# Kernel optimization log

Hardware: AMD Instinct MI355X
Metric: run time of the kernel (lower is better)

Reference implementation:

```python
import jax, jax.numpy as jnp
import numpy as np

N, E, D, H, C = 50000, 1600000, 256, 8, 32

def setup_inputs() -> dict:
    key = jax.random.key(0)
    ks = jax.random.split(key, 7)
    feat = jax.random.normal(ks[0], (N, D), dtype=jnp.float32)
    edge_weight = jax.random.uniform(ks[1], (E,), dtype=jnp.float32)
    W_lin = jax.random.normal(ks[2], (D, H * C), dtype=jnp.float32) * (1.0 / np.sqrt(D))
    att_l = jax.random.normal(ks[3], (1, H, C), dtype=jnp.float32) * (1.0 / np.sqrt(H))
    att_r = jax.random.normal(ks[4], (1, H, C), dtype=jnp.float32) * (1.0 / np.sqrt(H))
    W_res = jax.random.normal(ks[5], (D, H * C), dtype=jnp.float32) * (1.0 / np.sqrt(D))
    edge_index = jax.random.randint(ks[6], (2, E), 0, N, dtype=jnp.int32)
    return {"feat": feat, "edge_weight": edge_weight, "W_lin": W_lin,
            "att_l": att_l, "att_r": att_r, "W_res": W_res, "edge_index": edge_index}

def reference(feat, edge_weight, W_lin, att_l, att_r, W_res, edge_index):
    n_nodes = feat.shape[0]
    h, c = att_l.shape[1], att_l.shape[2]
    src, dst = edge_index[0], edge_index[1]
    # node projection: [N, H, C]
    x = (feat @ W_lin).reshape(n_nodes, h, c)
    alpha_l = (x * att_l).sum(-1)  # [N, H]
    alpha_r = (x * att_r).sum(-1)  # [N, H]
    # per-edge scores [E, H]
    alpha = alpha_l[src] + alpha_r[dst]
    alpha = edge_weight[:, None] * alpha
    alpha = jnp.where(alpha > 0, alpha, 0.2 * alpha)  # leaky_relu(0.2)
    # segment softmax over destination nodes
    amax = jax.lax.stop_gradient(jax.ops.segment_max(alpha, dst, num_segments=n_nodes))
    ex = jnp.exp(alpha - amax[dst])
    denom = jax.ops.segment_sum(ex, dst, num_segments=n_nodes)
    coeff = ex / (denom[dst] + 1e-16)  # [E, H]
    # weighted message aggregation
    msg = x[src] * coeff[:, :, None]  # [E, H, C]
    agg = jax.ops.segment_sum(msg, dst, num_segments=n_nodes)  # [N, H, C]
    out = jax.nn.elu(agg).reshape(n_nodes, h * c)
    out = out + feat @ W_res  # residual
    return out
```

## Files before the change

### kernel.cpp

```cpp
#include <hip/hip_runtime.h>
#include <stdint.h>

#define D_DIM 256
#define NPAD  640

typedef __bf16 bf16x8 __attribute__((ext_vector_type(8)));
typedef float  f32x4  __attribute__((ext_vector_type(4)));

__device__ __forceinline__ float bf2f(unsigned short u) {
  union { unsigned int i; float f; } cv; cv.i = ((unsigned int)u) << 16; return cv.f;
}
__device__ __forceinline__ unsigned short f2bf(float f) {
  union { float f; unsigned int i; } cv; cv.f = f;
  unsigned int i = cv.i;
  unsigned int lsb = (i >> 16) & 1u;
  i += 0x7fffu + lsb;
  return (unsigned short)(i >> 16);
}
__device__ __forceinline__ void gld16(const void* gptr, void* lptr) {
  __builtin_amdgcn_global_load_lds(
      (const __attribute__((address_space(1))) unsigned int*)gptr,
      (__attribute__((address_space(3))) unsigned int*)lptr, 16, 0, 0);
}

__global__ __launch_bounds__(256) void setup_cvt_prep(
    const float* __restrict__ feat, unsigned short* __restrict__ fb,
    const float* __restrict__ W_lin, const float* __restrict__ W_res,
    const float* __restrict__ att_l, const float* __restrict__ att_r,
    unsigned short* __restrict__ Bt, int nelem, int nb_cvt) {
  int bid = blockIdx.x, t = threadIdx.x;
  if (bid < nb_cvt) {
    int i = (bid * 256 + t) * 8;
    if (i >= nelem) return;
    float4 v0 = *(const float4*)(feat + i);
    float4 v1 = *(const float4*)(feat + i + 4);
    ushort4 a, b;
    a.x = f2bf(v0.x); a.y = f2bf(v0.y); a.z = f2bf(v0.z); a.w = f2bf(v0.w);
    b.x = f2bf(v1.x); b.y = f2bf(v1.y); b.z = f2bf(v1.z); b.w = f2bf(v1.w);
    *(ushort4*)(fb + i) = a;
    *(ushort4*)(fb + i + 4) = b;
  } else {
    int idx = (bid - nb_cvt) * 256 + t;
    int n = idx >> 8, k = idx & 255;
    float v = 0.f;
    if (n < 256) v = W_lin[k * 256 + n];
    else if (n < 512) v = W_res[k * 256 + (n - 256)];
    else if (n < 520) {
      int h = n - 512; float s = 0.f;
      #pragma unroll
      for (int c = 0; c < 32; ++c) s += W_lin[k * 256 + h * 32 + c] * att_l[h * 32 + c];
      v = s;
    } else if (n < 528) {
      int h = n - 520; float s = 0.f;
      #pragma unroll
      for (int c = 0; c < 32; ++c) s += W_lin[k * 256 + h * 32 + c] * att_r[h * 32 + c];
      v = s;
    }
    Bt[idx] = f2bf(v);
  }
}

__global__ __launch_bounds__(256) void scan_partial(const int* __restrict__ cnt,
                                                    int* __restrict__ bsum, int N) {
  __shared__ int s[256];
  int t = threadIdx.x;
  int i = blockIdx.x * 256 + t;
  s[t] = (i < N) ? cnt[i] : 0;
  __syncthreads();
  for (int off = 128; off > 0; off >>= 1) {
    if (t < off) s[t] += s[t + off];
    __syncthreads();
  }
  if (t == 0) bsum[blockIdx.x] = s[0];
}

__global__ __launch_bounds__(256) void scan_top(int* __restrict__ bsum, int nb) {
  __shared__ int s[256];
  int t = threadIdx.x;
  int v = (t < nb) ? bsum[t] : 0;
  s[t] = v;
  __syncthreads();
  for (int off = 1; off < 256; off <<= 1) {
    int u = (t >= off) ? s[t - off] : 0;
    __syncthreads();
    s[t] += u;
    __syncthreads();
  }
  if (t < nb) bsum[t] = s[t] - v;
}

__global__ __launch_bounds__(256) void scan_apply(const int* __restrict__ cnt,
                                                  const int* __restrict__ bsum,
                                                  int* __restrict__ row_ptr, int N) {
  __shared__ int s[256];
  int t = threadIdx.x;
  int i = blockIdx.x * 256 + t;
  int v = (i < N) ? cnt[i] : 0;
  s[t] = v;
  __syncthreads();
  for (int off = 1; off < 256; off <<= 1) {
    int u = (t >= off) ? s[t - off] : 0;
    __syncthreads();
    s[t] += u;
    __syncthreads();
  }
  int excl = bsum[blockIdx.x] + s[t] - v;
  if (i < N) {
    row_ptr[i] = excl;
    if (i == N - 1) row_ptr[N] = excl + v;
  }
}

__global__ __launch_bounds__(256) void gemm_hist(
    const unsigned short* __restrict__ A,
    const unsigned short* __restrict__ Bt,
    float* __restrict__ out, unsigned short* __restrict__ xbf,
    float* __restrict__ alpha_l, float* __restrict__ alpha_r, int M,
    const int* __restrict__ dst, int* __restrict__ cnt, int* __restrict__ rank,
    int E, int nb_hist, int gx) {
  __shared__ unsigned short As[128 * 64];
  __shared__ unsigned short Bs[128 * 64];

  if ((int)blockIdx.x < nb_hist) {
    int base = (int)blockIdx.x * 2048 + threadIdx.x;
    #pragma unroll
    for (int u = 0; u < 8; ++u) {
      int e = base + u * 256;
      if (e < E) rank[e] = atomicAdd(&cnt[dst[e]], 1);
    }
    return;
  }

  int tid  = threadIdx.x;
  int w    = tid >> 6, lane = tid & 63;
  int gb   = (int)blockIdx.x - nb_hist;
  int bm   = (gb % gx) * 128, bn = (gb / gx) * 128;
  int wm   = (w & 1) * 64, wn = (w >> 1) * 64;
  int l16  = lane & 15, quad = lane >> 4;

  f32x4 acc[4][4] = {};

  int sr8     = lane >> 3;
  int koff_sw = (((lane & 7) ^ sr8) * 8);

  for (int k0 = 0; k0 < 256; k0 += 64) {
    #pragma unroll
    for (int j = 0; j < 4; ++j) {
      int rbase = w * 32 + j * 8;
      int rga = bm + rbase + sr8; if (rga > M - 1) rga = M - 1;
      gld16(A  + (size_t)rga * 256 + k0 + koff_sw, &As[rbase * 64]);
      gld16(Bt + (size_t)(bn + rbase + sr8) * 256 + k0 + koff_sw, &Bs[rbase * 64]);
    }
    __syncthreads();
    #pragma unroll
    for (int kk = 0; kk < 64; kk += 32) {
      bf16x8 a[4], b[4];
      #pragma unroll
      for (int mi = 0; mi < 4; ++mi) {
        int r = wm + mi * 16 + l16;
        int col = (kk * 2 + quad * 16) ^ ((r & 7) << 4);
        a[mi] = *(const bf16x8*)((const char*)&As[r * 64] + col);
      }
      #pragma unroll
      for (int ni = 0; ni < 4; ++ni) {
        int r = wn + ni * 16 + l16;
        int col = (kk * 2 + quad * 16) ^ ((r & 7) << 4);
        b[ni] = *(const bf16x8*)((const char*)&Bs[r * 64] + col);
      }
      #pragma unroll
      for (int mi = 0; mi < 4; ++mi)
        #pragma unroll
        for (int ni = 0; ni < 4; ++ni)
          acc[mi][ni] = __builtin_amdgcn_mfma_f32_16x16x32_bf16(a[mi], b[ni], acc[mi][ni], 0, 0, 0);
    }
    __syncthreads();
  }

  #pragma unroll
  for (int mi = 0; mi < 4; ++mi) {
    #pragma unroll
    for (int r = 0; r < 4; ++r) {
      int row = bm + wm + mi * 16 + quad * 4 + r;
      if (row >= M) continue;
      #pragma unroll
      for (int ni = 0; ni < 4; ++ni) {
        int n = bn + wn + ni * 16 + l16;
        float v = acc[mi][ni][r];
        if (n < 256)      xbf[(size_t)row * 256 + n] = f2bf(v);
        else if (n < 512) out[(size_t)row * 256 + (n - 256)] = v;
        else if (n < 520) alpha_l[row * 8 + (n - 512)] = v;
        else if (n < 528) alpha_r[row * 8 + (n - 520)] = v;
      }
    }
  }
}

__global__ __launch_bounds__(256) void scatter_kernel(
    const int* __restrict__ eidx, const float* __restrict__ ew,
    const int* __restrict__ row_ptr, const int* __restrict__ rank,
    int2* __restrict__ pairs, int E) {
  int e = blockIdx.x * 256 + threadIdx.x;
  if (e < E) {
    int d = eidx[E + e];
    int pos = row_ptr[d] + rank[e];
    int2 p; p.x = eidx[e]; p.y = __float_as_int(ew[e]);
    pairs[pos] = p;
  }
}

__global__ __launch_bounds__(256) void agg_kernel(
    const int* __restrict__ row_ptr, const int2* __restrict__ pairs,
    const float* __restrict__ alpha_l, const float* __restrict__ alpha_r,
    const unsigned short* __restrict__ xbf, float* __restrict__ out, int N) {
  __shared__ float red[2][64][6];
  int nin  = threadIdx.x >> 7;
  int wv   = (threadIdx.x >> 6) & 1;
  int lane = threadIdx.x & 63;
  int node = blockIdx.x * 2 + nin;
  bool active = node < N;
  int h  = lane >> 3;
  int cb = lane << 2;

  float l = 0.f, ac0 = 0.f, ac1 = 0.f, ac2 = 0.f, ac3 = 0.f;

  if (active) {
    int beg = row_ptr[node], end = row_ptr[node + 1];
    if (beg < end) {
      float arv = alpha_r[node * 8 + h];
      int last = end - 1;
      const unsigned short* xb = xbf + cb;
      for (int jg = beg + wv * 4; jg < end; jg += 8) {
        int2 q[4];
        #pragma unroll
        for (int u = 0; u < 4; ++u) {
          int t = jg + u; t = (t < last) ? t : last;
          q[u] = pairs[t];
        }
        float al[4];
        #pragma unroll
        for (int u = 0; u < 4; ++u) al[u] = alpha_l[(size_t)q[u].x * 8 + h];
        ushort4 xv[4];
        #pragma unroll
        for (int u = 0; u < 4; ++u)
          xv[u] = *(const ushort4*)(xb + ((size_t)q[u].x << 8));
        #pragma unroll
        for (int u = 0; u < 4; ++u) {
          float a = __int_as_float(q[u].y) * (al[u] + arv);
          a = (a > 0.f) ? a : 0.2f * a;
          float p = __expf(a);
          p = (jg + u < end) ? p : 0.f;
          l += p;
          ac0 = fmaf(p, bf2f(xv[u].x), ac0);
          ac1 = fmaf(p, bf2f(xv[u].y), ac1);
          ac2 = fmaf(p, bf2f(xv[u].z), ac2);
          ac3 = fmaf(p, bf2f(xv[u].w), ac3);
        }
      }
    }
  }

  if (wv == 1) {
    red[nin][lane][0] = l;
    red[nin][lane][1] = ac0; red[nin][lane][2] = ac1;
    red[nin][lane][3] = ac2; red[nin][lane][4] = ac3;
  }
  __syncthreads();
  if (active && wv == 0) {
    l   += red[nin][lane][0];
    ac0 += red[nin][lane][1]; ac1 += red[nin][lane][2];
    ac2 += red[nin][lane][3]; ac3 += red[nin][lane][4];
    float r = 1.0f / (l + 1e-16f);
    float o0 = ac0 * r, o1 = ac1 * r, o2 = ac2 * r, o3 = ac3 * r;
    o0 = (o0 > 0.f) ? o0 : expm1f(o0);
    o1 = (o1 > 0.f) ? o1 : expm1f(o1);
    o2 = (o2 > 0.f) ? o2 : expm1f(o2);
    o3 = (o3 > 0.f) ? o3 : expm1f(o3);
    float4* op = (float4*)(out + ((size_t)node << 8) + cb);
    float4 res = *op;
    res.x += o0; res.y += o1; res.z += o2; res.w += o3;
    *op = res;
  }
}

extern "C" void kernel_launch(void* const* d_in, const int* in_sizes, int n_in,
                              void* d_out, int out_size, void* d_ws, size_t ws_size,
                              hipStream_t stream) {
  const float* feat  = (const float*)d_in[0];
  const float* ew    = (const float*)d_in[1];
  const float* W_lin = (const float*)d_in[2];
  const float* att_l = (const float*)d_in[3];
  const float* att_r = (const float*)d_in[4];
  const float* W_res = (const float*)d_in[5];
  const int*   eidx  = (const int*)d_in[6];
  float* out = (float*)d_out;

  int N = in_sizes[0] / D_DIM;
  int E = in_sizes[1];

  char* p = (char*)d_ws;
  auto alloc = [&](size_t bytes) {
    char* r = p; p += (bytes + 255) & ~(size_t)255; return r;
  };
  unsigned short* xbf  = (unsigned short*)alloc((size_t)N * 256 * 2);
  unsigned short* fb   = (unsigned short*)alloc((size_t)N * 256 * 2);
  float* alpha_l       = (float*)alloc((size_t)N * 8 * 4);
  float* alpha_r       = (float*)alloc((size_t)N * 8 * 4);
  unsigned short* Bt   = (unsigned short*)alloc((size_t)NPAD * D_DIM * 2);
  int*   row_ptr       = (int*)alloc((size_t)(N + 1) * 4);
  int*   cnt           = (int*)alloc((size_t)N * 4);
  int*   rank          = (int*)alloc((size_t)E * 4);
  int*   bsum          = (int*)alloc(1024);
  int2*  pairs_sep     = (int2*)alloc((size_t)E * 8);
  bool sep_ok = ((size_t)((char*)(pairs_sep + E) - (char*)d_ws) <= ws_size);
  int2* pairs = sep_ok ? pairs_sep : (int2*)fb;

  int nb      = (N + 255) / 256;
  int nb_cvt  = (N * 256 / 8 + 255) / 256;
  int nb_prep = NPAD * D_DIM / 256;
  int nb_hist = (E + 2047) / 2048;
  int nb_scat = (E + 255) / 256;
  int gx = (N + 127) / 128;
  int gemm_blocks = gx * (NPAD / 128);

  hipMemsetAsync(cnt, 0, (size_t)N * 4, stream);

  setup_cvt_prep<<<nb_cvt + nb_prep, 256, 0, stream>>>(
      feat, fb, W_lin, W_res, att_l, att_r, Bt, N * 256, nb_cvt);

  gemm_hist<<<nb_hist + gemm_blocks, 256, 0, stream>>>(
      fb, Bt, out, xbf, alpha_l, alpha_r, N,
      eidx + E, cnt, rank, E, nb_hist, gx);

  scan_partial<<<nb, 256, 0, stream>>>(cnt, bsum, N);
  scan_top<<<1, 256, 0, stream>>>(bsum, nb);
  scan_apply<<<nb, 256, 0, stream>>>(cnt, bsum, row_ptr, N);

  scatter_kernel<<<nb_scat, 256, 0, stream>>>(eidx, ew, row_ptr, rank, pairs, E);

  agg_kernel<<<(N + 1) / 2, 256, 0, stream>>>(row_ptr, pairs, alpha_l, alpha_r, xbf, out, N);
}
```

Baseline: 408.7 us.

## Precompute per-edge exp scores in a separate kernel and split hist from GEMM

Adds a score kernel that computes the leaky-relu exp attention weights for all 8 heads once per edge in CSR order and stores them as bf16. The aggregation kernel then reads these instead of gathering alpha_l per lane and evaluating exp per lane. This needs a per-edge dst array, which scan_apply fills serially per node. The histogram is also split back out of the fused GEMM kernel into its own launch. The trade is the cost of writing and reading an extra E x 8 bf16 buffer, plus bf16 rounding of the softmax weights.

Measured after the change: 420.4 us. 1.03x slower.

```diff
diff --git a/kernel.cpp b/kernel.cpp
--- a/kernel.cpp
+++ b/kernel.cpp
@@ -60,6 +60,16 @@
   }
 }
 
+__global__ __launch_bounds__(256) void hist_kernel(
+    const int* __restrict__ dst, int* __restrict__ cnt, int* __restrict__ rank, int E) {
+  int base = (int)blockIdx.x * 2048 + threadIdx.x;
+  #pragma unroll
+  for (int u = 0; u < 8; ++u) {
+    int e = base + u * 256;
+    if (e < E) rank[e] = atomicAdd(&cnt[dst[e]], 1);
+  }
+}
+
 __global__ __launch_bounds__(256) void scan_partial(const int* __restrict__ cnt,
                                                     int* __restrict__ bsum, int N) {
   __shared__ int s[256];
@@ -91,7 +101,8 @@
 
 __global__ __launch_bounds__(256) void scan_apply(const int* __restrict__ cnt,
                                                   const int* __restrict__ bsum,
-                                                  int* __restrict__ row_ptr, int N) {
+                                                  int* __restrict__ row_ptr,
+                                                  int* __restrict__ dstA, int mode, int N) {
   __shared__ int s[256];
   int t = threadIdx.x;
   int i = blockIdx.x * 256 + t;
@@ -107,33 +118,25 @@
   int excl = bsum[blockIdx.x] + s[t] - v;
   if (i < N) {
     row_ptr[i] = excl;
+    if (mode) {
+      int e2 = excl + v;
+      for (int j = excl; j < e2; ++j) dstA[j] = i;
+    }
     if (i == N - 1) row_ptr[N] = excl + v;
   }
 }
 
-__global__ __launch_bounds__(256) void gemm_hist(
+__global__ __launch_bounds__(256) void gemm_kernel(
     const unsigned short* __restrict__ A,
     const unsigned short* __restrict__ Bt,
     float* __restrict__ out, unsigned short* __restrict__ xbf,
-    float* __restrict__ alpha_l, float* __restrict__ alpha_r, int M,
-    const int* __restrict__ dst, int* __restrict__ cnt, int* __restrict__ rank,
-    int E, int nb_hist, int gx) {
+    float* __restrict__ alpha_l, float* __restrict__ alpha_r, int M, int gx) {
   __shared__ unsigned short As[128 * 64];
   __shared__ unsigned short Bs[128 * 64];
 
-  if ((int)blockIdx.x < nb_hist) {
-    int base = (int)blockIdx.x * 2048 + threadIdx.x;
-    #pragma unroll
-    for (int u = 0; u < 8; ++u) {
-      int e = base + u * 256;
-      if (e < E) rank[e] = atomicAdd(&cnt[dst[e]], 1);
-    }
-    return;
-  }
-
   int tid  = threadIdx.x;
   int w    = tid >> 6, lane = tid & 63;
-  int gb   = (int)blockIdx.x - nb_hist;
+  int gb   = (int)blockIdx.x;
   int bm   = (gb % gx) * 128, bn = (gb / gx) * 128;
   int wm   = (w & 1) * 64, wn = (w >> 1) * 64;
   int l16  = lane & 15, quad = lane >> 4;
@@ -208,10 +211,40 @@
   }
 }
 
+__global__ __launch_bounds__(256) void score_kernel(
+    const int2* __restrict__ pairs, const int* __restrict__ dstA,
+    const float* __restrict__ alpha_l, const float* __restrict__ alpha_r,
+    unsigned short* __restrict__ pexp, int E) {
+  int t = blockIdx.x * 256 + threadIdx.x;
+  if (t >= E) return;
+  int2 pr = pairs[t];
+  int d = dstA[t];
+  float w = __int_as_float(pr.y);
+  float4 al0 = *(const float4*)(alpha_l + (size_t)pr.x * 8);
+  float4 al1 = *(const float4*)(alpha_l + (size_t)pr.x * 8 + 4);
+  float4 ar0 = *(const float4*)(alpha_r + (size_t)d * 8);
+  float4 ar1 = *(const float4*)(alpha_r + (size_t)d * 8 + 4);
+  float a[8] = {al0.x + ar0.x, al0.y + ar0.y, al0.z + ar0.z, al0.w + ar0.w,
+                al1.x + ar1.x, al1.y + ar1.y, al1.z + ar1.z, al1.w + ar1.w};
+  unsigned short pb[8];
+  #pragma unroll
+  for (int h = 0; h < 8; ++h) {
+    float v = w * a[h];
+    v = (v > 0.f) ? v : 0.2f * v;
+    pb[h] = f2bf(__expf(v));
+  }
+  ushort4 o0, o1;
+  o0.x = pb[0]; o0.y = pb[1]; o0.z = pb[2]; o0.w = pb[3];
+  o1.x = pb[4]; o1.y = pb[5]; o1.z = pb[6]; o1.w = pb[7];
+  *(ushort4*)(pexp + (size_t)t * 8) = o0;
+  *(ushort4*)(pexp + (size_t)t * 8 + 4) = o1;
+}
+
 __global__ __launch_bounds__(256) void agg_kernel(
     const int* __restrict__ row_ptr, const int2* __restrict__ pairs,
+    const unsigned short* __restrict__ pexp,
     const float* __restrict__ alpha_l, const float* __restrict__ alpha_r,
-    const unsigned short* __restrict__ xbf, float* __restrict__ out, int N) {
+    const unsigned short* __restrict__ xbf, float* __restrict__ out, int mode, int N) {
   __shared__ float red[2][64][6];
   int nin  = threadIdx.x >> 7;
   int wv   = (threadIdx.x >> 6) & 1;
@@ -226,34 +259,59 @@
   if (active) {
     int beg = row_ptr[node], end = row_ptr[node + 1];
     if (beg < end) {
-      float arv = alpha_r[node * 8 + h];
       int last = end - 1;
       const unsigned short* xb = xbf + cb;
-      for (int jg = beg + wv * 4; jg < end; jg += 8) {
-        int2 q[4];
-        #pragma unroll
-        for (int u = 0; u < 4; ++u) {
-          int t = jg + u; t = (t < last) ? t : last;
-          q[u] = pairs[t];
+      if (mode) {
+        for (int jg = beg + wv * 4; jg < end; jg += 8) {
+          int s[4]; float pv[4];
+          #pragma unroll
+          for (int u = 0; u < 4; ++u) {
+            int t = jg + u; t = (t < last) ? t : last;
+            s[u]  = pairs[t].x;
+            pv[u] = bf2f(pexp[(size_t)t * 8 + h]);
+          }
+          ushort4 xv[4];
+          #pragma unroll
+          for (int u = 0; u < 4; ++u)
+            xv[u] = *(const ushort4*)(xb + ((size_t)s[u] << 8));
+          #pragma unroll
+          for (int u = 0; u < 4; ++u) {
+            float p = (jg + u < end) ? pv[u] : 0.f;
+            l += p;
+            ac0 = fmaf(p, bf2f(xv[u].x), ac0);
+            ac1 = fmaf(p, bf2f(xv[u].y), ac1);
+            ac2 = fmaf(p, bf2f(xv[u].z), ac2);
+            ac3 = fmaf(p, bf2f(xv[u].w), ac3);
+          }
         }
-        float al[4];
-        #pragma unroll
-        for (int u = 0; u < 4; ++u) al[u] = alpha_l[(size_t)q[u].x * 8 + h];
-        ushort4 xv[4];
-        #pragma unroll
-        for (int u = 0; u < 4; ++u)
-          xv[u] = *(const ushort4*)(xb + ((size_t)q[u].x << 8));
-        #pragma unroll
-        for (int u = 0; u < 4; ++u) {
-          float a = __int_as_float(q[u].y) * (al[u] + arv);
-          a = (a > 0.f) ? a : 0.2f * a;
-          float p = __expf(a);
-          p = (jg + u < end) ? p : 0.f;
-          l += p;
-          ac0 = fmaf(p, bf2f(xv[u].x), ac0);
-          ac1 = fmaf(p, bf2f(xv[u].y), ac1);
-          ac2 = fmaf(p, bf2f(xv[u].z), ac2);
-          ac3 = fmaf(p, bf2f(xv[u].w), ac3);
+      } else {
+        float arv = alpha_r[node * 8 + h];
+        for (int jg = beg + wv * 4; jg < end; jg += 8) {
+          int2 q[4];
+          #pragma unroll
+          for (int u = 0; u < 4; ++u) {
+            int t = jg + u; t = (t < last) ? t : last;
+            q[u] = pairs[t];
+          }
+          float al[4];
+          #pragma unroll
+          for (int u = 0; u < 4; ++u) al[u] = alpha_l[(size_t)q[u].x * 8 + h];
+          ushort4 xv[4];
+          #pragma unroll
+          for (int u = 0; u < 4; ++u)
+            xv[u] = *(const ushort4*)(xb + ((size_t)q[u].x << 8));
+          #pragma unroll
+          for (int u = 0; u < 4; ++u) {
+            float a = __int_as_float(q[u].y) * (al[u] + arv);
+            a = (a > 0.f) ? a : 0.2f * a;
+            float p = __expf(a);
+            p = (jg + u < end) ? p : 0.f;
+            l += p;
+            ac0 = fmaf(p, bf2f(xv[u].x), ac0);
+            ac1 = fmaf(p, bf2f(xv[u].y), ac1);
+            ac2 = fmaf(p, bf2f(xv[u].z), ac2);
+            ac3 = fmaf(p, bf2f(xv[u].w), ac3);
+          }
         }
       }
     }
@@ -310,9 +368,22 @@
   int*   cnt           = (int*)alloc((size_t)N * 4);
   int*   rank          = (int*)alloc((size_t)E * 4);
   int*   bsum          = (int*)alloc(1024);
-  int2*  pairs_sep     = (int2*)alloc((size_t)E * 8);
-  bool sep_ok = ((size_t)((char*)(pairs_sep + E) - (char*)d_ws) <= ws_size);
-  int2* pairs = sep_ok ? pairs_sep : (int2*)fb;
+  int2*  pairs         = (int2*)alloc((size_t)E * 8);
+  char*  opt_base      = p;
+  int*   dstA          = (int*)alloc((size_t)E * 4);
+  unsigned short* pexp = (unsigned short*)alloc((size_t)E * 8 * 2);
+
+  int mode = 1;
+  if ((size_t)(p - (char*)d_ws) > ws_size) {
+    p = opt_base;
+    dstA = (int*)alloc((size_t)E * 4);
+    pexp = fb;
+    if ((size_t)(p - (char*)d_ws) > ws_size) {
+      mode = 0;
+      if ((size_t)((char*)(pairs + E) - (char*)d_ws) > ws_size)
+        pairs = (int2*)fb;
+    }
+  }
 
   int nb      = (N + 255) / 256;
   int nb_cvt  = (N * 256 / 8 + 255) / 256;
@@ -327,15 +398,20 @@
   setup_cvt_prep<<<nb_cvt + nb_prep, 256, 0, stream>>>(
       feat, fb, W_lin, W_res, att_l, att_r, Bt, N * 256, nb_cvt);
 
-  gemm_hist<<<nb_hist + gemm_blocks, 256, 0, stream>>>(
-      fb, Bt, out, xbf, alpha_l, alpha_r, N,
-      eidx + E, cnt, rank, E, nb_hist, gx);
+  hist_kernel<<<nb_hist, 256, 0, stream>>>(eidx + E, cnt, rank, E);
+
+  gemm_kernel<<<gemm_blocks, 256, 0, stream>>>(
+      fb, Bt, out, xbf, alpha_l, alpha_r, N, gx);
 
   scan_partial<<<nb, 256, 0, stream>>>(cnt, bsum, N);
   scan_top<<<1, 256, 0, stream>>>(bsum, nb);
-  scan_apply<<<nb, 256, 0, stream>>>(cnt, bsum, row_ptr, N);
+  scan_apply<<<nb, 256, 0, stream>>>(cnt, bsum, row_ptr, dstA, mode, N);
 
   scatter_kernel<<<nb_scat, 256, 0, stream>>>(eidx, ew, row_ptr, rank, pairs, E);
 
-  agg_kernel<<<(N + 1) / 2, 256, 0, stream>>>(row_ptr, pairs, alpha_l, alpha_r, xbf, out, N);
-}
+  if (mode)
+    score_kernel<<<nb_scat, 256, 0, stream>>>(pairs, dstA, alpha_l, alpha_r, pexp, E);
+
+  agg_kernel<<<(N + 1) / 2, 256, 0, stream>>>(
+      row_ptr, pairs, pexp, alpha_l, alpha_r, xbf, out, mode, N);
+}
```
